# Optimization experiments

Measured on AMD Instinct MI355X. Metric: run time of the kernel, lower is better.

The kernel has to match this reference:

```python
import jax, jax.numpy as jnp
import numpy as np

B, S, I, H = 8, 512, 512, 512
L, NH = 2, 8
N_MEM, W_MEM = 1024, 64
FF = 4 * H
HD = H // NH
# interface layout: read keys | read betas | write key | write beta | erase | write vec | write gate
D_IF = NH * W_MEM + NH + W_MEM + 1 + W_MEM + W_MEM + 1


def setup_inputs():
    key = jax.random.key(0)
    ks = jax.random.split(key, 10)
    g = lambda k, sh, s=0.02: jax.random.normal(k, sh, dtype=jnp.float32) * s
    return dict(
        x=jax.random.normal(ks[0], (B, S, I), dtype=jnp.float32),
        Wp=g(ks[1], (I, H)), bp=jnp.zeros((H,), jnp.float32),
        Wqkv=g(ks[2], (L, H, 3 * H)), bqkv=jnp.zeros((L, 3 * H), jnp.float32),
        Wo=g(ks[3], (L, H, H)), bo=jnp.zeros((L, H), jnp.float32),
        ln1_g=jnp.ones((L, H), jnp.float32), ln1_b=jnp.zeros((L, H), jnp.float32),
        W1=g(ks[4], (L, H, FF)), b1=jnp.zeros((L, FF), jnp.float32),
        W2=g(ks[5], (L, FF, H)), b2=jnp.zeros((L, H), jnp.float32),
        ln2_g=jnp.ones((L, H), jnp.float32), ln2_b=jnp.zeros((L, H), jnp.float32),
        Wi=g(ks[6], (H, D_IF)), bi=jnp.zeros((D_IF,), jnp.float32),
        M0=g(ks[7], (N_MEM, W_MEM), 0.01),
    )


def _ln(x, g, b):
    m = jnp.mean(x, -1, keepdims=True)
    v = jnp.var(x, -1, keepdims=True)
    return (x - m) * jax.lax.rsqrt(v + 1e-5) * g + b


def _encoder(h, Wqkv, bqkv, Wo, bo, ln1_g, ln1_b, W1, b1, W2, b2, ln2_g, ln2_b):
    for l in range(L):  # small fixed layer count
        qkv = h @ Wqkv[l] + bqkv[l]
        q, k, v = jnp.split(qkv, 3, axis=-1)
        to_heads = lambda t: t.reshape(B, S, NH, HD).transpose(0, 2, 1, 3)
        q, k, v = to_heads(q), to_heads(k), to_heads(v)
        att = jax.nn.softmax(jnp.einsum('bhqd,bhkd->bhqk', q, k) / np.float32(np.sqrt(HD)), -1)
        o = jnp.einsum('bhqk,bhkd->bhqd', att, v).transpose(0, 2, 1, 3).reshape(B, S, H)
        h = _ln(h + o @ Wo[l] + bo[l], ln1_g[l], ln1_b[l])
        ff = jax.nn.relu(h @ W1[l] + b1[l]) @ W2[l] + b2[l]
        h = _ln(h + ff, ln2_g[l], ln2_b[l])
    return h


def _cos_addr(M, k, beta):
    # M: [B, N, W]; k: [B, ..., W]; beta: [B, ...] -> softmax weights over N slots
    Mn = M * jax.lax.rsqrt(jnp.sum(M * M, -1, keepdims=True) + 1e-8)
    kn = k * jax.lax.rsqrt(jnp.sum(k * k, -1, keepdims=True) + 1e-8)
    sim = jnp.einsum('bnw,...w->...n', Mn, kn) if False else jnp.einsum('bnw,b...w->b...n', Mn, kn)
    return jax.nn.softmax(beta[..., None] * sim, -1)


def _dnc_memory(iface, M0):
    # iface: [B, S, D_IF]
    o = NH * W_MEM
    rk = iface[..., :o].reshape(B, S, NH, W_MEM)
    rb = jax.nn.softplus(iface[..., o:o + NH]); o += NH
    wk = iface[..., o:o + W_MEM]; o += W_MEM
    wb = jax.nn.softplus(iface[..., o]); o += 1
    er = jax.nn.sigmoid(iface[..., o:o + W_MEM]); o += W_MEM
    wv = iface[..., o:o + W_MEM]; o += W_MEM
    gw = jax.nn.sigmoid(iface[..., o])
    xs = (jnp.swapaxes(wk, 0, 1), wb.T, jnp.swapaxes(er, 0, 1),
          jnp.swapaxes(wv, 0, 1), gw.T, jnp.swapaxes(rk, 0, 1), jnp.swapaxes(rb, 0, 1))
    M_init = jnp.broadcast_to(M0, (B, N_MEM, W_MEM))

    def step(M, t):
        wk_t, wb_t, e_t, v_t, g_t, rk_t, rb_t = t
        ww = g_t[:, None] * _cos_addr(M, wk_t, wb_t)                         # [B, N]
        M = M * (1.0 - ww[:, :, None] * e_t[:, None, :]) + ww[:, :, None] * v_t[:, None, :]
        rw = _cos_addr(M, rk_t, rb_t)                                        # [B, NH, N]
        r = jnp.einsum('bhn,bnw->bhw', rw, M).reshape(B, NH * W_MEM)
        return M, r

    _, reads = jax.lax.scan(step, M_init, xs)
    return jnp.swapaxes(reads, 0, 1)  # [B, S, NH*W_MEM]


def reference(x, Wp, bp, Wqkv, bqkv, Wo, bo, ln1_g, ln1_b, W1, b1, W2, b2, ln2_g, ln2_b, Wi, bi, M0):
    h = x @ Wp + bp  # input_projection
    tout = _encoder(h, Wqkv, bqkv, Wo, bo, ln1_g, ln1_b, W1, b1, W2, b2, ln2_g, ln2_b)
    iface = tout @ Wi + bi
    read_vector = _dnc_memory(iface, M0)
    return (tout, read_vector)
```

## Files before the change

kernel.cpp:

```cpp
#include <hip/hip_runtime.h>

typedef unsigned short u16;
typedef unsigned int u32;
typedef __attribute__((ext_vector_type(8))) short s16x8;
typedef __attribute__((ext_vector_type(8))) u16 u16x8;
typedef __attribute__((ext_vector_type(4))) u16 u16x4;
typedef __attribute__((ext_vector_type(4))) u32 u32x4;
typedef __attribute__((ext_vector_type(4))) float f32x4;
typedef __attribute__((ext_vector_type(2))) float f32x2;

#define L2E 1.4426950408889634f

__device__ __forceinline__ u16 f2bf(float f) {
  unsigned u = __builtin_bit_cast(unsigned, f);
  u = (u + 0x7fffu + ((u >> 16) & 1u)) >> 16;
  return (u16)u;
}
__device__ __forceinline__ float bf2f(u16 s) {
  unsigned u = ((unsigned)s) << 16;
  return __builtin_bit_cast(float, u);
}
__device__ __forceinline__ float blo(u32 d) { return __builtin_bit_cast(float, d << 16); }
__device__ __forceinline__ float bhi(u32 d) { return __builtin_bit_cast(float, d & 0xFFFF0000u); }
__device__ __forceinline__ float sigmoidf_(float x) { return 1.f / (1.f + __expf(-x)); }
__device__ __forceinline__ float softplusf_(float x) { return (x > 20.f) ? x : logf(1.f + __expf(x)); }

__device__ __forceinline__ f32x2 pk_fma_vvv(f32x2 a, f32x2 b, f32x2 c) {
  f32x2 d;
  asm("v_pk_fma_f32 %0, %1, %2, %3" : "=v"(d) : "v"(a), "v"(b), "v"(c));
  return d;
}
__device__ __forceinline__ f32x2 pk_fma_svv(f32x2 a, f32x2 b, f32x2 c) {
  f32x2 d;
  asm("v_pk_fma_f32 %0, %1, %2, %3" : "=v"(d) : "s"(a), "v"(b), "v"(c));
  return d;
}

template <int CTRL, int RMASK>
__device__ __forceinline__ float dpp_add(float v) {
  int x = __builtin_amdgcn_update_dpp(0, __builtin_bit_cast(int, v), CTRL, RMASK, 0xf, true);
  return v + __builtin_bit_cast(float, x);
}
__device__ __forceinline__ float wred_sum_dpp(float v) {
  v = dpp_add<0x111, 0xf>(v);
  v = dpp_add<0x112, 0xf>(v);
  v = dpp_add<0x114, 0xf>(v);
  v = dpp_add<0x118, 0xf>(v);
  v = dpp_add<0x142, 0xa>(v);
  v = dpp_add<0x143, 0xc>(v);
  return __builtin_bit_cast(float, __builtin_amdgcn_readlane(__builtin_bit_cast(int, v), 63));
}

__device__ __forceinline__ float wred_sum(float v) {
  #pragma unroll
  for (int d = 1; d < 64; d <<= 1) v += __shfl_xor(v, d);
  return v;
}
__device__ __forceinline__ float wred_max(float v) {
  #pragma unroll
  for (int d = 1; d < 64; d <<= 1) v = fmaxf(v, __shfl_xor(v, d));
  return v;
}

__global__ void castx_k(const float* __restrict__ in, u16* __restrict__ out, int n4) {
  int i = blockIdx.x * 256 + threadIdx.x;
  if (i < n4) {
    f32x4 v = *(const f32x4*)(in + (long)i * 4);
    u16x4 o;
    o.x = f2bf(v.x); o.y = f2bf(v.y); o.z = f2bf(v.z); o.w = f2bf(v.w);
    *(u16x4*)(out + (long)i * 4) = o;
  }
}

__global__ void castT_k(const float* __restrict__ in, u16* __restrict__ out, int K, int N) {
  long base = (long)blockIdx.z * K * N;
  int idx = blockIdx.x * 256 + threadIdx.x;
  if (idx < K * N) {
    int n = idx / K, k = idx - n * K;
    out[base + idx] = f2bf(in[base + (long)k * N + n]);
  }
}

__global__ void vtx_k(const u16* __restrict__ qkv, u16* __restrict__ vT) {
  int idx = blockIdx.x * 256 + threadIdx.x;
  int s = idx & 511;
  int d = (idx >> 9) & 63;
  int bh = idx >> 15;
  int b = bh >> 3, h = bh & 7;
  vT[idx] = qkv[((long)(b * 512 + s)) * 1536 + 1024 + h * 64 + d];
}

struct GemmP {
  const u16* A; const u16* B; const float* bias;
  float* outF; u16* outB;
  int M, N, K, lda, ldb, ldc;
  long sAb, sAh, sAz, sBb, sBh, sBz, sCb, sCh, sCz;
  int zdiv, z0;
  float alpha; int relu;
};

__global__ __launch_bounds__(256) void gemm_k(GemmP p) {
  __shared__ u16 sA[128 * 72];
  __shared__ u16 sB[128 * 72];
  int tid = threadIdx.x;
  int gp = p.z0 + blockIdx.z;
  int zb = gp / p.zdiv, zh = gp - zb * p.zdiv;
  const u16* Ab = p.A + zb * p.sAb + zh * p.sAh + (long)blockIdx.z * p.sAz + (long)blockIdx.x * 128 * p.lda;
  const u16* Bb = p.B + zb * p.sBb + zh * p.sBh + (long)blockIdx.z * p.sBz;
  long coff = zb * p.sCb + zh * p.sCh + (long)blockIdx.z * p.sCz;
  int bn = blockIdx.y * 128;
  int lane = tid & 63, wid = tid >> 6;
  int wr = wid >> 1, wc = wid & 1;

  f32x4 acc[4][4];
  f32x4 z4 = {0.f, 0.f, 0.f, 0.f};
  #pragma unroll
  for (int i = 0; i < 4; i++)
    #pragma unroll
    for (int j = 0; j < 4; j++) acc[i][j] = z4;

  int r = tid >> 1, c32 = (tid & 1) * 32;
  for (int k0 = 0; k0 < p.K; k0 += 64) {
    const u16* Ag = Ab + (long)r * p.lda + k0 + c32;
    u16x8* dA = (u16x8*)(sA + r * 72 + c32);
    #pragma unroll
    for (int i = 0; i < 4; i++) dA[i] = *(const u16x8*)(Ag + i * 8);
    int nrow = bn + r;
    u16x8* dB = (u16x8*)(sB + r * 72 + c32);
    if (nrow < p.N) {
      const u16* Bg = Bb + (long)nrow * p.ldb + k0 + c32;
      #pragma unroll
      for (int i = 0; i < 4; i++) dB[i] = *(const u16x8*)(Bg + i * 8);
    } else {
      u16x8 zz = (u16x8)0;
      #pragma unroll
      for (int i = 0; i < 4; i++) dB[i] = zz;
    }
    __syncthreads();
    #pragma unroll
    for (int ks = 0; ks < 2; ks++) {
      int ko = ks * 32 + (lane >> 4) * 8;
      s16x8 af[4], bf[4];
      #pragma unroll
      for (int m = 0; m < 4; m++) af[m] = *(const s16x8*)(sA + (wr * 64 + m * 16 + (lane & 15)) * 72 + ko);
      #pragma unroll
      for (int n = 0; n < 4; n++) bf[n] = *(const s16x8*)(sB + (wc * 64 + n * 16 + (lane & 15)) * 72 + ko);
      #pragma unroll
      for (int m = 0; m < 4; m++)
        #pragma unroll
        for (int n = 0; n < 4; n++)
          acc[m][n] = __builtin_amdgcn_mfma_f32_16x16x32_bf16(af[m], bf[n], acc[m][n], 0, 0, 0);
    }
    __syncthreads();
  }

  int row0 = blockIdx.x * 128 + wr * 64;
  int col0 = bn + wc * 64;
  #pragma unroll
  for (int n = 0; n < 4; n++) {
    int col = col0 + n * 16 + (lane & 15);
    if (col >= p.N) continue;
    float bv = p.bias ? p.bias[col] : 0.f;
    #pragma unroll
    for (int m = 0; m < 4; m++) {
      #pragma unroll
      for (int q = 0; q < 4; q++) {
        int row = row0 + m * 16 + (lane >> 4) * 4 + q;
        float v = acc[m][n][q] * p.alpha + bv;
        if (p.relu) v = fmaxf(v, 0.f);
        long ci = coff + (long)row * p.ldc + col;
        if (p.outF) p.outF[ci] = v;
        if (p.outB) p.outB[ci] = f2bf(v);
      }
    }
  }
}

__global__ __launch_bounds__(64) void ln_k(const float* __restrict__ a, const float* __restrict__ res,
                                           const float* __restrict__ g, const float* __restrict__ bb,
                                           float* __restrict__ outF, u16* __restrict__ outB) {
  int row = blockIdx.x, t = threadIdx.x;
  const float* ar = a + (long)row * 512;
  const float* rr = res + (long)row * 512;
  float x[8];
  float s1 = 0.f;
  #pragma unroll
  for (int i = 0; i < 8; i++) { x[i] = ar[i * 64 + t] + rr[i * 64 + t]; s1 += x[i]; }
  s1 = wred_sum(s1);
  float mean = s1 * (1.f / 512.f);
  float s2 = 0.f;
  #pragma unroll
  for (int i = 0; i < 8; i++) { float d = x[i] - mean; s2 += d * d; }
  s2 = wred_sum(s2);
  float inv = rsqrtf(s2 * (1.f / 512.f) + 1e-5f);
  #pragma unroll
  for (int i = 0; i < 8; i++) {
    int cc = i * 64 + t;
    float y = (x[i] - mean) * inv * g[cc] + bb[cc];
    outF[(long)row * 512 + cc] = y;
    outB[(long)row * 512 + cc] = f2bf(y);
  }
}

__global__ __launch_bounds__(64) void smaxb_k(u16* __restrict__ p) {
  long row = blockIdx.x;
  u16* pr = p + row * 512;
  int t = threadIdx.x;
  u16x8 v = *(const u16x8*)(pr + t * 8);
  float f[8];
  float mx = -1e30f;
  #pragma unroll
  for (int i = 0; i < 8; i++) { f[i] = bf2f(v[i]); mx = fmaxf(mx, f[i]); }
  mx = wred_max(mx);
  float se = 0.f;
  #pragma unroll
  for (int i = 0; i < 8; i++) { f[i] = __expf(f[i] - mx); se += f[i]; }
  se = wred_sum(se);
  float inv = __builtin_amdgcn_rcpf(se);
  #pragma unroll
  for (int i = 0; i < 8; i++) v[i] = f2bf(f[i] * inv);
  *(u16x8*)(pr + t * 8) = v;
}

__global__ __launch_bounds__(256) void prep_k(const float* __restrict__ iface,
                                              float* __restrict__ rec1,
                                              float* __restrict__ rec2) {
  int idx = blockIdx.x * 4 + (threadIdx.x >> 6);
  int lane = threadIdx.x & 63;
  const float* r = iface + (long)idx * 714;
  float* o1 = rec1 + ((long)idx << 8);
  float* o2 = rec2 + ((long)idx << 9);
  float wk = r[520 + lane];
  float s2k = wred_sum(wk * wk);
  float wb = softplusf_(r[584]);
  o1[lane] = wk * (wb * L2E * rsqrtf(s2k + 1e-8f));
  o1[64 + lane] = -sigmoidf_(r[585 + lane]);
  o1[128 + lane] = r[649 + lane];
  #pragma unroll
  for (int h = 0; h < 8; h++) {
    float rk = r[h * 64 + lane];
    float s2r = wred_sum(rk * rk);
    float rb = softplusf_(r[512 + h]);
    o2[h * 64 + lane] = rk * (rb * L2E * rsqrtf(s2r + 1e-8f));
  }
  if (!lane) o1[192] = sigmoidf_(r[713]);
}

__global__ __launch_bounds__(1024, 4) void scan1_k(const float* __restrict__ rec1,
                                                   const float* __restrict__ M0,
                                                   float* __restrict__ ww_out,
                                                   u16* __restrict__ snap) {
  int b = blockIdx.x, tid = threadIdx.x, lane = tid & 63, wid = tid >> 6;
  __shared__ float s_red[2][16];
  f32x2 m[32];
  {
    const float* M0r = M0 + (long)tid * 64;
    #pragma unroll
    for (int i = 0; i < 32; i++) m[i] = *(const f32x2*)(M0r + i * 2);
  }
  const float* rb_ = rec1 + ((long)b << 17);
  float* wwb = ww_out + (long)b * 512 * 1024;
  u16* snb = snap + (long)b * 2097152;

  for (int t8 = 0; t8 < 64; ++t8) {
    if ((t8 & 1) == 0) {
      u16* sr = snb + ((long)(t8 >> 1) * 1024 + tid) * 64;
      #pragma unroll
      for (int i = 0; i < 8; i++) {
        u16x8 o;
        #pragma unroll
        for (int j = 0; j < 8; j++) { int e = i * 8 + j; o[j] = f2bf(m[e >> 1][e & 1]); }
        *(u16x8*)(sr + i * 8) = o;
      }
    }
    float wwreg[8];
    #pragma unroll
    for (int j = 0; j < 8; ++j) {
      int t = t8 * 8 + j;
      const float* kr = rb_ + ((long)t << 8);
      f32x2 n0 = {1e-8f, 0.f}, n1 = {0.f, 0.f};
      f32x2 d0 = {0.f, 0.f}, d1 = {0.f, 0.f};
      #pragma unroll
      for (int i = 0; i < 32; i += 2) {
        f32x2 k0 = *(const f32x2*)(kr + i * 2);
        f32x2 k1 = *(const f32x2*)(kr + i * 2 + 2);
        n0 = pk_fma_vvv(m[i], m[i], n0);
        d0 = pk_fma_svv(k0, m[i], d0);
        n1 = pk_fma_vvv(m[i + 1], m[i + 1], n1);
        d1 = pk_fma_svv(k1, m[i + 1], d1);
      }
      float n2 = (n0.x + n0.y) + (n1.x + n1.y);
      float dot = (d0.x + d0.y) + (d1.x + d1.y);
      float ew = __builtin_amdgcn_exp2f(dot * rsqrtf(n2));
      float ws = wred_sum_dpp(ew);
      if (!lane) s_red[j & 1][wid] = ws;
      __syncthreads();
      float tot;
      {
        const f32x4* rr = (const f32x4*)&s_red[j & 1][0];
        f32x4 a = rr[0], bq = rr[1], cq = rr[2], dq = rr[3];
        tot = ((a.x + a.y) + (a.z + a.w)) + ((bq.x + bq.y) + (bq.z + bq.w)) +
              ((cq.x + cq.y) + (cq.z + cq.w)) + ((dq.x + dq.y) + (dq.z + dq.w));
      }
      float ww = kr[192] * ew * __builtin_amdgcn_rcpf(tot);
      wwreg[j] = ww;
      f32x2 ww2 = {ww, ww};
      #pragma unroll
      for (int i = 0; i < 32; i++) {
        f32x2 ne = *(const f32x2*)(kr + 64 + i * 2);
        f32x2 vv = *(const f32x2*)(kr + 128 + i * 2);
        f32x2 tt = pk_fma_svv(ne, m[i], vv);
        m[i] = pk_fma_vvv(ww2, tt, m[i]);
      }
    }
    #pragma unroll
    for (int j = 0; j < 8; ++j)
      wwb[(long)(t8 * 8 + j) * 1024 + tid] = wwreg[j];
  }
}

#define P2_LDS 148480
__global__ __launch_bounds__(1024, 4) void scan2_k(const float* __restrict__ rec1,
                                                   const float* __restrict__ rec2,
                                                   const float* __restrict__ ww_in,
                                                   const u16* __restrict__ snap,
                                                   float* __restrict__ out) {
  int b = blockIdx.x, c = blockIdx.y, tid = threadIdx.x, lane = tid & 63, wid = tid >> 6;
  extern __shared__ char smem[];
  u16* s_Mbf = (u16*)smem;
  u16* s_rw = s_Mbf + 65536;
  float* s_red = (float*)(s_rw + 8192);

  f32x2 m[32];
  {
    const u16* sr = snap + (((long)b * 32 + c) * 1024 + tid) * 64;
    #pragma unroll
    for (int i = 0; i < 8; i++) {
      u16x8 v = *(const u16x8*)(sr + i * 8);
      #pragma unroll
      for (int j = 0; j < 8; j++) { int e = i * 8 + j; m[e >> 1][e & 1] = bf2f(v[j]); }
    }
  }
  const float* rb1 = rec1 + ((long)b << 17);
  const float* rb2 = rec2 + ((long)b << 18);
  const float* wwb = ww_in + (long)b * 512 * 1024;
  float* outb = out + (long)b * 512 * 512;
  int t0 = c * 16;
  int n7 = tid & 7;
  int blkswz = tid ^ ((tid >> 3) & 7);

  for (int ti = 0; ti < 16; ++ti) {
    int t = t0 + ti, cb = ti & 1;
    const float* kr1 = rb1 + ((long)t << 8);
    const float* kr2 = rb2 + ((long)t << 9);
    float ww = wwb[(long)t * 1024 + tid];
    __syncthreads();

    f32x2 ww2 = {ww, ww};
    f32x2 nn0 = {1e-8f, 0.f}, nn1 = {0.f, 0.f};
    #pragma unroll
    for (int i = 0; i < 32; i++) {
      f32x2 ne = *(const f32x2*)(kr1 + 64 + i * 2);
      f32x2 vv = *(const f32x2*)(kr1 + 128 + i * 2);
      f32x2 tt = pk_fma_svv(ne, m[i], vv);
      f32x2 mv = pk_fma_vvv(ww2, tt, m[i]);
      m[i] = mv;
      if (i & 1) nn1 = pk_fma_vvv(mv, mv, nn1);
      else       nn0 = pk_fma_vvv(mv, mv, nn0);
    }
    float invm = rsqrtf((nn0.x + nn0.y) + (nn1.x + nn1.y));
    #pragma unroll
    for (int i = 0; i < 8; i++) {
      u16x8 o;
      #pragma unroll
      for (int j = 0; j < 8; j++) { int e = i * 8 + j; o[j] = f2bf(m[e >> 1][e & 1]); }
      *(u16x8*)(s_Mbf + tid * 64 + ((i ^ n7) << 3)) = o;
    }
    float eh[8];
    u16x8 ehb;
    #pragma unroll
    for (int h = 0; h < 8; h++) {
      f32x2 a0 = {0.f, 0.f}, a1 = {0.f, 0.f};
      #pragma unroll
      for (int i = 0; i < 32; i += 2) {
        f32x2 k0 = *(const f32x2*)(kr2 + h * 64 + i * 2);
        f32x2 k1 = *(const f32x2*)(kr2 + h * 64 + i * 2 + 2);
        a0 = pk_fma_svv(k0, m[i], a0);
        a1 = pk_fma_svv(k1, m[i + 1], a1);
      }
      float d = (a0.x + a0.y) + (a1.x + a1.y);
      eh[h] = __builtin_amdgcn_exp2f(d * invm);
      ehb[h] = f2bf(eh[h]);
    }
    *(u16x8*)(s_rw + (blkswz << 3)) = ehb;
    #pragma unroll
    for (int h = 0; h < 8; h++) {
      float sh = wred_sum_dpp(eh[h]);
      if (!lane) s_red[cb * 128 + wid * 8 + h] = sh;
    }
    __syncthreads();

    float p[8];
    #pragma unroll
    for (int h = 0; h < 8; h++) p[h] = 0.f;
    int rbase = wid << 6;
    int cblk = lane >> 3, cin = lane & 7;
    #pragma unroll 4
    for (int j = 0; j < 64; j++) {
      int r = rbase + j;
      float mf = bf2f(s_Mbf[(r << 6) + (((cblk ^ r) & 7) << 3) + cin]);
      int rsw = r ^ ((r >> 3) & 7);
      u32x4 rr = *(const u32x4*)(s_rw + (rsw << 3));
      p[0] = __builtin_fmaf(mf, blo(rr.x), p[0]); p[1] = __builtin_fmaf(mf, bhi(rr.x), p[1]);
      p[2] = __builtin_fmaf(mf, blo(rr.y), p[2]); p[3] = __builtin_fmaf(mf, bhi(rr.y), p[3]);
      p[4] = __builtin_fmaf(mf, blo(rr.z), p[4]); p[5] = __builtin_fmaf(mf, bhi(rr.z), p[5]);
      p[6] = __builtin_fmaf(mf, blo(rr.w), p[6]); p[7] = __builtin_fmaf(mf, bhi(rr.w), p[7]);
    }
    {
      float* pbw = (float*)(s_Mbf + (wid << 12));
      #pragma unroll
      for (int h = 0; h < 8; h++) pbw[h * 64 + lane] = p[h];
    }
    __syncthreads();

    if (tid < 512) {
      int h = tid >> 6, ow = tid & 63;
      float s = 0.f;
      #pragma unroll
      for (int j = 0; j < 16; j++) s += ((const float*)(s_Mbf + (j << 12)))[h * 64 + ow];
      float tt = 0.f;
      #pragma unroll
      for (int j = 0; j < 16; j++) tt += s_red[cb * 128 + j * 8 + h];
      outb[(long)t * 512 + tid] = s * __builtin_amdgcn_rcpf(tt);
    }
  }
}

static void launch_gemm(hipStream_t stream, const u16* A, int lda, const u16* B, int ldb,
                        const float* bias, float* oF, u16* oB, int ldc,
                        int M, int N, int K, int gz,
                        long sAb, long sAh, long sAz, long sBb, long sBh, long sBz,
                        long sCb, long sCh, long sCz, int zdiv, int z0, float alpha, int relu) {
  GemmP p;
  p.A = A; p.B = B; p.bias = bias; p.outF = oF; p.outB = oB;
  p.M = M; p.N = N; p.K = K; p.lda = lda; p.ldb = ldb; p.ldc = ldc;
  p.sAb = sAb; p.sAh = sAh; p.sAz = sAz;
  p.sBb = sBb; p.sBh = sBh; p.sBz = sBz;
  p.sCb = sCb; p.sCh = sCh; p.sCz = sCz;
  p.zdiv = zdiv; p.z0 = z0; p.alpha = alpha; p.relu = relu;
  dim3 g(M / 128, (N + 127) / 128, gz);
  gemm_k<<<g, 256, 0, stream>>>(p);
}

extern "C" void kernel_launch(void* const* d_in, const int* in_sizes, int n_in,
                              void* d_out, int out_size, void* d_ws, size_t ws_size,
                              hipStream_t stream) {
  (void)in_sizes; (void)n_in; (void)out_size; (void)ws_size;
  const float* x    = (const float*)d_in[0];
  const float* Wp   = (const float*)d_in[1];
  const float* bp   = (const float*)d_in[2];
  const float* Wqkv = (const float*)d_in[3];
  const float* bqkv = (const float*)d_in[4];
  const float* Wo   = (const float*)d_in[5];
  const float* bo   = (const float*)d_in[6];
  const float* ln1g = (const float*)d_in[7];
  const float* ln1b = (const float*)d_in[8];
  const float* W1   = (const float*)d_in[9];
  const float* b1   = (const float*)d_in[10];
  const float* W2   = (const float*)d_in[11];
  const float* b2   = (const float*)d_in[12];
  const float* ln2g = (const float*)d_in[13];
  const float* ln2b = (const float*)d_in[14];
  const float* Wi   = (const float*)d_in[15];
  const float* bi   = (const float*)d_in[16];
  const float* M0   = (const float*)d_in[17];
  float* outF = (float*)d_out;

  char* ws = (char*)d_ws;
  u16* WpT   = (u16*)ws;
  u16* WqkvT = WpT + 262144;
  u16* WoT   = WqkvT + 1572864;
  u16* W1T   = WoT + 524288;
  u16* W2T   = W1T + 2097152;
  u16* WiT   = W2T + 2097152;
  u16* xb    = WiT + 365568;
  u16* hb    = xb + 2097152;
  float* h   = (float*)(hb + 2097152);
  u16* qkvb  = (u16*)(h + 2097152);
  u16* vT    = qkvb + 6291456;
  float* scores = (float*)(vT + 2097152);
  u16* pbuf  = (u16*)(scores + 4194304);
  u16* obuf  = pbuf + 4194304;
  float* gout = (float*)(obuf + 2097152);
  u16* ffb   = (u16*)(gout + 2924544);
  float* ifbuf = (float*)(ffb + 8388608);
  u16* scoresB = (u16*)gout;
  float* prepb1 = (float*)qkvb;
  float* prepb2 = prepb1 + 1048576;
  float* wwbuf = scores;
  u16* snapb  = pbuf;

  castx_k<<<2048, 256, 0, stream>>>(x, xb, 524288);
  castT_k<<<dim3(1024, 1, 1), 256, 0, stream>>>(Wp, WpT, 512, 512);
  castT_k<<<dim3(3072, 1, 2), 256, 0, stream>>>(Wqkv, WqkvT, 512, 1536);
  castT_k<<<dim3(1024, 1, 2), 256, 0, stream>>>(Wo, WoT, 512, 512);
  castT_k<<<dim3(4096, 1, 2), 256, 0, stream>>>(W1, W1T, 512, 2048);
  castT_k<<<dim3(4096, 1, 2), 256, 0, stream>>>(W2, W2T, 2048, 512);
  castT_k<<<dim3(1428, 1, 1), 256, 0, stream>>>(Wi, WiT, 512, 714);

  launch_gemm(stream, xb, 512, WpT, 512, bp, h, hb, 512, 4096, 512, 512,
              1, 0,0,0, 0,0,0, 0,0,0, 1, 0, 1.f, 0);

  for (int l = 0; l < 2; ++l) {
    launch_gemm(stream, hb, 512, WqkvT + (long)l * 786432, 512, bqkv + l * 1536,
                nullptr, qkvb, 1536, 4096, 1536, 512,
                1, 0,0,0, 0,0,0, 0,0,0, 1, 0, 1.f, 0);
    vtx_k<<<8192, 256, 0, stream>>>(qkvb, vT);
    launch_gemm(stream, qkvb, 1536, qkvb + 512, 1536, nullptr, nullptr, scoresB, 512,
                512, 512, 64, 64,
                786432, 64, 0,  786432, 64, 0,  2097152, 262144, 0, 8, 0, 0.125f, 0);
    smaxb_k<<<32768, 64, 0, stream>>>(scoresB);
    launch_gemm(stream, scoresB, 512, vT, 512, nullptr, nullptr, obuf, 512,
                512, 64, 512, 64,
                2097152, 262144, 0,  262144, 32768, 0,  262144, 64, 0, 8, 0, 1.f, 0);
    launch_gemm(stream, obuf, 512, WoT + (long)l * 262144, 512, bo + l * 512,
                gout, nullptr, 512, 4096, 512, 512,
                1, 0,0,0, 0,0,0, 0,0,0, 1, 0, 1.f, 0);
    ln_k<<<4096, 64, 0, stream>>>(gout, h, ln1g + l * 512, ln1b + l * 512, h, hb);
    launch_gemm(stream, hb, 512, W1T + (long)l * 1048576, 512, b1 + l * 2048,
                nullptr, ffb, 2048, 4096, 2048, 512,
                1, 0,0,0, 0,0,0, 0,0,0, 1, 0, 1.f, 1);
    launch_gemm(stream, ffb, 2048, W2T + (long)l * 1048576, 2048, b2 + l * 512,
                gout, nullptr, 512, 4096, 512, 2048,
                1, 0,0,0, 0,0,0, 0,0,0, 1, 0, 1.f, 0);
    float* lnout = (l == 1) ? outF : h;
    ln_k<<<4096, 64, 0, stream>>>(gout, h, ln2g + l * 512, ln2b + l * 512, lnout, hb);
  }

  launch_gemm(stream, hb, 512, WiT, 512, bi, ifbuf, nullptr, 714,
              4096, 714, 512, 1, 0,0,0, 0,0,0, 0,0,0, 1, 0, 1.f, 0);

  prep_k<<<1024, 256, 0, stream>>>(ifbuf, prepb1, prepb2);
  scan1_k<<<8, 1024, 0, stream>>>(prepb1, M0, wwbuf, snapb);
  hipFuncSetAttribute(reinterpret_cast<const void*>(scan2_k),
                      hipFuncAttributeMaxDynamicSharedMemorySize, P2_LDS);
  scan2_k<<<dim3(8, 32), 1024, P2_LDS, stream>>>(prepb1, prepb2, wwbuf, snapb, outF + 2097152);
}
```

Measured before the change: 2.327 ms.

## Fuse memory scan passes into one kernel with progress-flag producer/consumer overlap

Merges the sequential write-weight scan and the chunked read scan into a single launch. Block role 0 per batch runs the serial scan and publishes a per-batch progress counter with release atomics every 16 steps. The other blocks spin on that counter with acquire loads, then replay their 16-step chunk from the bf16 snapshot, so read work overlaps the serial scan instead of waiting for it to finish. This relies on all 256 blocks being co-resident to avoid deadlock. It also adds spin-wait cost and a memset of the counters.

```diff
diff --git a/kernel.cpp b/kernel.cpp
--- a/kernel.cpp
+++ b/kernel.cpp
@@ -246,91 +246,106 @@
   if (!lane) o1[192] = sigmoidf_(r[713]);
 }
 
-__global__ __launch_bounds__(1024, 4) void scan1_k(const float* __restrict__ rec1,
+#define P2_LDS 148480
+__global__ __launch_bounds__(1024, 4) void fused_k(const float* __restrict__ rec1,
+                                                   const float* __restrict__ rec2,
                                                    const float* __restrict__ M0,
                                                    float* __restrict__ ww_out,
-                                                   u16* __restrict__ snap) {
-  int b = blockIdx.x, tid = threadIdx.x, lane = tid & 63, wid = tid >> 6;
-  __shared__ float s_red[2][16];
-  f32x2 m[32];
-  {
-    const float* M0r = M0 + (long)tid * 64;
-    #pragma unroll
-    for (int i = 0; i < 32; i++) m[i] = *(const f32x2*)(M0r + i * 2);
-  }
-  const float* rb_ = rec1 + ((long)b << 17);
-  float* wwb = ww_out + (long)b * 512 * 1024;
-  u16* snb = snap + (long)b * 2097152;
-
-  for (int t8 = 0; t8 < 64; ++t8) {
-    if ((t8 & 1) == 0) {
-      u16* sr = snb + ((long)(t8 >> 1) * 1024 + tid) * 64;
-      #pragma unroll
-      for (int i = 0; i < 8; i++) {
-        u16x8 o;
-        #pragma unroll
-        for (int j = 0; j < 8; j++) { int e = i * 8 + j; o[j] = f2bf(m[e >> 1][e & 1]); }
-        *(u16x8*)(sr + i * 8) = o;
-      }
-    }
-    float wwreg[8];
-    #pragma unroll
-    for (int j = 0; j < 8; ++j) {
-      int t = t8 * 8 + j;
-      const float* kr = rb_ + ((long)t << 8);
-      f32x2 n0 = {1e-8f, 0.f}, n1 = {0.f, 0.f};
-      f32x2 d0 = {0.f, 0.f}, d1 = {0.f, 0.f};
-      #pragma unroll
-      for (int i = 0; i < 32; i += 2) {
-        f32x2 k0 = *(const f32x2*)(kr + i * 2);
-        f32x2 k1 = *(const f32x2*)(kr + i * 2 + 2);
-        n0 = pk_fma_vvv(m[i], m[i], n0);
-        d0 = pk_fma_svv(k0, m[i], d0);
-        n1 = pk_fma_vvv(m[i + 1], m[i + 1], n1);
-        d1 = pk_fma_svv(k1, m[i + 1], d1);
-      }
-      float n2 = (n0.x + n0.y) + (n1.x + n1.y);
-      float dot = (d0.x + d0.y) + (d1.x + d1.y);
-      float ew = __builtin_amdgcn_exp2f(dot * rsqrtf(n2));
-      float ws = wred_sum_dpp(ew);
-      if (!lane) s_red[j & 1][wid] = ws;
-      __syncthreads();
-      float tot;
-      {
-        const f32x4* rr = (const f32x4*)&s_red[j & 1][0];
-        f32x4 a = rr[0], bq = rr[1], cq = rr[2], dq = rr[3];
-        tot = ((a.x + a.y) + (a.z + a.w)) + ((bq.x + bq.y) + (bq.z + bq.w)) +
-              ((cq.x + cq.y) + (cq.z + cq.w)) + ((dq.x + dq.y) + (dq.z + dq.w));
-      }
-      float ww = kr[192] * ew * __builtin_amdgcn_rcpf(tot);
-      wwreg[j] = ww;
-      f32x2 ww2 = {ww, ww};
-      #pragma unroll
-      for (int i = 0; i < 32; i++) {
-        f32x2 ne = *(const f32x2*)(kr + 64 + i * 2);
-        f32x2 vv = *(const f32x2*)(kr + 128 + i * 2);
-        f32x2 tt = pk_fma_svv(ne, m[i], vv);
-        m[i] = pk_fma_vvv(ww2, tt, m[i]);
-      }
-    }
-    #pragma unroll
-    for (int j = 0; j < 8; ++j)
-      wwb[(long)(t8 * 8 + j) * 1024 + tid] = wwreg[j];
-  }
-}
-
-#define P2_LDS 148480
-__global__ __launch_bounds__(1024, 4) void scan2_k(const float* __restrict__ rec1,
-                                                   const float* __restrict__ rec2,
-                                                   const float* __restrict__ ww_in,
-                                                   const u16* __restrict__ snap,
-                                                   float* __restrict__ out) {
-  int b = blockIdx.x, c = blockIdx.y, tid = threadIdx.x, lane = tid & 63, wid = tid >> 6;
+                                                   u16* __restrict__ snap,
+                                                   float* __restrict__ out,
+                                                   u32* __restrict__ prog) {
+  int b = blockIdx.x, role = blockIdx.y;
+  int tid = threadIdx.x, lane = tid & 63, wid = tid >> 6;
   extern __shared__ char smem[];
   u16* s_Mbf = (u16*)smem;
   u16* s_rw = s_Mbf + 65536;
   float* s_red = (float*)(s_rw + 8192);
 
+  const float* rb1 = rec1 + ((long)b << 17);
+  const float* rb2 = rec2 + ((long)b << 18);
+  float* wwb = ww_out + (long)b * 512 * 1024;
+  u16* snb = snap + (long)b * 2097152;
+  float* outb = out + (long)b * 512 * 512;
+
+  if (role == 0) {
+    f32x2 m[32];
+    {
+      const float* M0r = M0 + (long)tid * 64;
+      #pragma unroll
+      for (int i = 0; i < 32; i++) m[i] = *(const f32x2*)(M0r + i * 2);
+    }
+    for (int t8 = 0; t8 < 64; ++t8) {
+      if ((t8 & 1) == 0) {
+        u16* sr = snb + ((long)(t8 >> 1) * 1024 + tid) * 64;
+        #pragma unroll
+        for (int i = 0; i < 8; i++) {
+          u16x8 o;
+          #pragma unroll
+          for (int j = 0; j < 8; j++) { int e = i * 8 + j; o[j] = f2bf(m[e >> 1][e & 1]); }
+          *(u16x8*)(sr + i * 8) = o;
+        }
+      }
+      float wwreg[8];
+      #pragma unroll
+      for (int j = 0; j < 8; ++j) {
+        int t = t8 * 8 + j;
+        const float* kr = rb1 + ((long)t << 8);
+        f32x2 n0 = {1e-8f, 0.f}, n1 = {0.f, 0.f};
+        f32x2 d0 = {0.f, 0.f}, d1 = {0.f, 0.f};
+        #pragma unroll
+        for (int i = 0; i < 32; i += 2) {
+          f32x2 k0 = *(const f32x2*)(kr + i * 2);
+          f32x2 k1 = *(const f32x2*)(kr + i * 2 + 2);
+          n0 = pk_fma_vvv(m[i], m[i], n0);
+          d0 = pk_fma_svv(k0, m[i], d0);
+          n1 = pk_fma_vvv(m[i + 1], m[i + 1], n1);
+          d1 = pk_fma_svv(k1, m[i + 1], d1);
+        }
+        float n2 = (n0.x + n0.y) + (n1.x + n1.y);
+        float dot = (d0.x + d0.y) + (d1.x + d1.y);
+        float ew = __builtin_amdgcn_exp2f(dot * rsqrtf(n2));
+        float ws = wred_sum_dpp(ew);
+        if (!lane) s_red[(j & 1) * 16 + wid] = ws;
+        __syncthreads();
+        float tot;
+        {
+          const f32x4* rr = (const f32x4*)&s_red[(j & 1) * 16];
+          f32x4 a = rr[0], bq = rr[1], cq = rr[2], dq = rr[3];
+          tot = ((a.x + a.y) + (a.z + a.w)) + ((bq.x + bq.y) + (bq.z + bq.w)) +
+                ((cq.x + cq.y) + (cq.z + cq.w)) + ((dq.x + dq.y) + (dq.z + dq.w));
+        }
+        float ww = kr[192] * ew * __builtin_amdgcn_rcpf(tot);
+        wwreg[j] = ww;
+        f32x2 ww2 = {ww, ww};
+        #pragma unroll
+        for (int i = 0; i < 32; i++) {
+          f32x2 ne = *(const f32x2*)(kr + 64 + i * 2);
+          f32x2 vv = *(const f32x2*)(kr + 128 + i * 2);
+          f32x2 tt = pk_fma_svv(ne, m[i], vv);
+          m[i] = pk_fma_vvv(ww2, tt, m[i]);
+        }
+      }
+      #pragma unroll
+      for (int j = 0; j < 8; ++j)
+        wwb[(long)(t8 * 8 + j) * 1024 + tid] = wwreg[j];
+      if (t8 & 1) {
+        __syncthreads();
+        if (tid == 0)
+          __hip_atomic_store(prog + b, (u32)((t8 + 1) >> 1),
+                             __ATOMIC_RELEASE, __HIP_MEMORY_SCOPE_AGENT);
+      }
+    }
+    __syncthreads();
+  } else {
+    if (tid == 0) {
+      while (__hip_atomic_load(prog + b, __ATOMIC_ACQUIRE, __HIP_MEMORY_SCOPE_AGENT)
+             < (u32)(role + 1))
+        __builtin_amdgcn_s_sleep(16);
+    }
+    __syncthreads();
+  }
+
+  int c = role;
   f32x2 m[32];
   {
     const u16* sr = snap + (((long)b * 32 + c) * 1024 + tid) * 64;
@@ -341,10 +356,6 @@
       for (int j = 0; j < 8; j++) { int e = i * 8 + j; m[e >> 1][e & 1] = bf2f(v[j]); }
     }
   }
-  const float* rb1 = rec1 + ((long)b << 17);
-  const float* rb2 = rec2 + ((long)b << 18);
-  const float* wwb = ww_in + (long)b * 512 * 1024;
-  float* outb = out + (long)b * 512 * 512;
   int t0 = c * 16;
   int n7 = tid & 7;
   int blkswz = tid ^ ((tid >> 3) & 7);
@@ -499,6 +510,7 @@
   float* prepb2 = prepb1 + 1048576;
   float* wwbuf = scores;
   u16* snapb  = pbuf;
+  u32* progb  = (u32*)vT;
 
   castx_k<<<2048, 256, 0, stream>>>(x, xb, 524288);
   castT_k<<<dim3(1024, 1, 1), 256, 0, stream>>>(Wp, WpT, 512, 512);
@@ -541,8 +553,9 @@
               4096, 714, 512, 1, 0,0,0, 0,0,0, 0,0,0, 1, 0, 1.f, 0);
 
   prep_k<<<1024, 256, 0, stream>>>(ifbuf, prepb1, prepb2);
-  scan1_k<<<8, 1024, 0, stream>>>(prepb1, M0, wwbuf, snapb);
-  hipFuncSetAttribute(reinterpret_cast<const void*>(scan2_k),
+  hipMemsetAsync(progb, 0, 8 * sizeof(u32), stream);
+  hipFuncSetAttribute(reinterpret_cast<const void*>(fused_k),
                       hipFuncAttributeMaxDynamicSharedMemorySize, P2_LDS);
-  scan2_k<<<dim3(8, 32), 1024, P2_LDS, stream>>>(prepb1, prepb2, wwbuf, snapb, outF + 2097152);
-}
+  fused_k<<<dim3(8, 32), 1024, P2_LDS, stream>>>(prepb1, prepb2, M0, wwbuf, snapb,
+                                                 outF + 2097152, progb);
+}
```

Result: slower. 6.133 ms (+163.6%).
